# Kernel optimization log

Hardware: AMD Instinct MI355X
Metric: run time of the kernel (lower is better)

Reference implementation:

```python
import jax, jax.numpy as jnp
import numpy as np

NUM_HEADS = 8
NUM_GROUPS = 32
EPS = 1e-5


def setup_inputs() -> dict:
    key = jax.random.key(0)
    ks = jax.random.split(key, 5)
    B, C, H, W = 8, 512, 32, 32
    x = jax.random.normal(ks[0], (B, C, H, W), dtype=jnp.float32)
    norm_w = jnp.ones((C,), dtype=jnp.float32)
    norm_b = jnp.zeros((C,), dtype=jnp.float32)
    qkv_w = jax.random.normal(ks[1], (3 * C, C), dtype=jnp.float32) * (1.0 / np.sqrt(C))
    qkv_b = jax.random.normal(ks[2], (3 * C,), dtype=jnp.float32) * 0.02
    proj_w = jax.random.normal(ks[3], (C, C), dtype=jnp.float32) * (1.0 / np.sqrt(C))
    proj_b = jax.random.normal(ks[4], (C,), dtype=jnp.float32) * 0.02
    return {"x": x, "norm_w": norm_w, "norm_b": norm_b,
            "qkv_w": qkv_w, "qkv_b": qkv_b, "proj_w": proj_w, "proj_b": proj_b}


def _group_norm(x, w, b):
    # x: [B, C, T]; normalize over (C//G, T) per group
    B, C, T = x.shape
    xg = x.reshape(B, NUM_GROUPS, (C // NUM_GROUPS) * T)
    mean = xg.mean(axis=-1, keepdims=True)
    var = xg.var(axis=-1, keepdims=True)
    xn = ((xg - mean) * jax.lax.rsqrt(var + EPS)).reshape(B, C, T)
    return xn * w[None, :, None] + b[None, :, None]


def reference(x, norm_w, norm_b, qkv_w, qkv_b, proj_w, proj_b):
    B, C, H, W = x.shape
    T = H * W
    x3 = x.reshape(B, C, T)
    h = _group_norm(x3, norm_w, norm_b)
    # 1x1 conv == channel matmul: [B, 3C, T]
    qkv = jnp.einsum('oc,bct->bot', qkv_w, h) + qkv_b[None, :, None]
    nh = NUM_HEADS
    ch = C // nh
    qkv = qkv.reshape(B * nh, 3 * ch, T)
    q, k, v = jnp.split(qkv, 3, axis=1)  # each [B*nh, ch, T]
    scale = 1.0 / np.sqrt(np.sqrt(ch))
    w = jnp.einsum('bct,bcs->bts', q * scale, k * scale)  # [B*nh, T, T]
    w = jax.nn.softmax(w, axis=-1)
    a = jnp.einsum('bts,bcs->bct', w, v).reshape(B, C, T)
    out = jnp.einsum('oc,bct->bot', proj_w, a) + proj_b[None, :, None]
    return (x3 + out).reshape(B, C, H, W)
```

## Files before the change

kernel.cpp:

```cpp
#include <hip/hip_runtime.h>
#include <stdint.h>

typedef short v8s __attribute__((ext_vector_type(8)));
typedef float v4f __attribute__((ext_vector_type(4)));

#define MFMA(a, b, c) __builtin_amdgcn_mfma_f32_16x16x32_bf16((a), (b), (c), 0, 0, 0)

__device__ __forceinline__ short f2bf(float f) {
  union { float f; uint32_t u; } v; v.f = f;
  uint32_t r = v.u + 0x7fffu + ((v.u >> 16) & 1u);
  return (short)(r >> 16);
}

__device__ __forceinline__ uint32_t pack2(float a, float b) {
  union { float f; uint32_t u; } ua, ub; ua.f = a; ub.f = b;
  return __builtin_amdgcn_perm(ub.u, ua.u, 0x07060302u);
}

__device__ __forceinline__ void gload16(const void* g, void* l) {
  __builtin_amdgcn_global_load_lds((const __attribute__((address_space(1))) void*)g,
                                   (__attribute__((address_space(3))) void*)l,
                                   16, 0, 0);
}

__global__ __launch_bounds__(256) void prep_gn_kernel(
    const float* __restrict__ qkvw, const float* __restrict__ qkvb,
    const float* __restrict__ projw,
    short* __restrict__ Wq, short* __restrict__ Wp, float* __restrict__ bias2,
    const float* __restrict__ x, const float* __restrict__ gw,
    const float* __restrict__ gb, short* __restrict__ hT) {
  __shared__ float red[8];
  __shared__ short tile[16 * 1032];
  int tid = threadIdx.x;
  if (blockIdx.x >= 256) {
    int idx = (blockIdx.x - 256) * 256 + tid;
    if (idx < 1536 * 512) {
      int r = idx >> 9, c = idx & 511;
      int sec = r >> 9;
      int rr = r & 511;
      int nh = rr >> 6, cc = rr & 63;
      int o = nh * 192 + sec * 64 + cc;
      Wq[idx] = f2bf(qkvw[o * 512 + c]);
      if (c == 0) bias2[r] = qkvb[o];
    } else {
      int j = idx - 1536 * 512;
      if (j < 512 * 512) Wp[j] = f2bf(projw[j]);
    }
    return;
  }
  int b = blockIdx.x >> 5, g = blockIdx.x & 31;
  const float* xg = x + (b * 512 + g * 16) * 1024;
  float s = 0.f, ss = 0.f;
#pragma unroll
  for (int r = 0; r < 16; ++r) {
    float4 v = *(const float4*)(xg + r * 1024 + tid * 4);
    s += v.x + v.y + v.z + v.w;
    ss += v.x * v.x + v.y * v.y + v.z * v.z + v.w * v.w;
  }
#pragma unroll
  for (int off = 32; off > 0; off >>= 1) {
    s += __shfl_xor(s, off, 64);
    ss += __shfl_xor(ss, off, 64);
  }
  if ((tid & 63) == 0) { red[tid >> 6] = s; red[4 + (tid >> 6)] = ss; }
  __syncthreads();
  float S = red[0] + red[1] + red[2] + red[3];
  float SS = red[4] + red[5] + red[6] + red[7];
  float mean = S * (1.f / 16384.f);
  float var = SS * (1.f / 16384.f) - mean * mean;
  float inv = rsqrtf(var + 1e-5f);
#pragma unroll
  for (int r = 0; r < 16; ++r) {
    int c = g * 16 + r;
    float a = inv * gw[c];
    float bb = gb[c] - mean * a;
    float4 v = *(const float4*)(xg + r * 1024 + tid * 4);
    short* tr = tile + r * 1032 + tid * 4;
    tr[0] = f2bf(fmaf(v.x, a, bb));
    tr[1] = f2bf(fmaf(v.y, a, bb));
    tr[2] = f2bf(fmaf(v.z, a, bb));
    tr[3] = f2bf(fmaf(v.w, a, bb));
  }
  __syncthreads();
  int r = tid & 15, tq = tid >> 4;
  int c = g * 16 + r;
  short* dst = hT + b * 1024 * 512 + c;
  const short* src = tile + r * 1032;
#pragma unroll
  for (int i = 0; i < 64; ++i) {
    int t = i * 16 + tq;
    dst[t * 512] = src[t];
  }
}

__device__ __forceinline__ void gemm_k512_b64(
    const short* __restrict__ Ag, const short* __restrict__ Bg,
    short* lA, short* lB, int wid, int lane, v4f acc[4][4]) {
  int wr = (wid >> 1) * 64, wc = (wid & 1) * 64;
  int c16 = lane & 15, q = lane >> 4;
  int srow = lane >> 3;
  int sw = ((lane & 7) ^ srow) * 8;
  const short* gaw = Ag + (wid * 32 + srow) * 512 + sw;
  const short* gbw = Bg + (wid * 32 + srow) * 512 + sw;
  short* lAw = lA + wid * 2048;
  short* lBw = lB + wid * 2048;
  int pc0 = (q ^ (c16 & 7)) * 8;
  int pc1 = ((4 + q) ^ (c16 & 7)) * 8;
  for (int kt = 0; kt < 8; ++kt) {
    int k0 = kt * 64;
#pragma unroll
    for (int t = 0; t < 4; ++t)
      gload16(gaw + t * 8 * 512 + k0, lAw + t * 512);
#pragma unroll
    for (int t = 0; t < 4; ++t)
      gload16(gbw + t * 8 * 512 + k0, lBw + t * 512);
    __syncthreads();
#pragma unroll
    for (int ks = 0; ks < 2; ++ks) {
      int pc = ks ? pc1 : pc0;
      v8s af[4], bf[4];
#pragma unroll
      for (int i = 0; i < 4; ++i)
        af[i] = *(const v8s*)(lA + (wr + i * 16 + c16) * 64 + pc);
#pragma unroll
      for (int j = 0; j < 4; ++j)
        bf[j] = *(const v8s*)(lB + (wc + j * 16 + c16) * 64 + pc);
#pragma unroll
      for (int i = 0; i < 4; ++i)
#pragma unroll
        for (int j = 0; j < 4; ++j)
          acc[i][j] = MFMA(af[i], bf[j], acc[i][j]);
    }
    __syncthreads();
  }
}

__global__ __launch_bounds__(256) void qkv_gemm_kernel(
    const short* __restrict__ hT, const short* __restrict__ Wq,
    const float* __restrict__ bias2,
    short* __restrict__ Qb, short* __restrict__ Kb, short* __restrict__ Vb) {
  __shared__ __align__(16) short smem[17408];
  short* lA = smem;
  short* lB = smem + 8192;
  short* vt = smem;
  int bm = blockIdx.x & 63, bo = blockIdx.x >> 6;
  int tid = threadIdx.x, wid = tid >> 6, lane = tid & 63;
  int wr = (wid >> 1) * 64, wc = (wid & 1) * 64;
  int q = lane >> 4, c16 = lane & 15;
  v4f acc[4][4];
#pragma unroll
  for (int i = 0; i < 4; ++i)
#pragma unroll
    for (int j = 0; j < 4; ++j) acc[i][j] = (v4f){0.f, 0.f, 0.f, 0.f};
  gemm_k512_b64(hT + bm * 128 * 512, Wq + bo * 128 * 512, lA, lB, wid, lane, acc);
  float bv[4];
#pragma unroll
  for (int j = 0; j < 4; ++j) bv[j] = bias2[bo * 128 + wc + j * 16 + c16];
  if (bo < 8) {
    short* dst = (bo < 4) ? Qb : Kb;
    float sc = (bo < 4) ? 0.18033688f : 1.f;
#pragma unroll
    for (int j = 0; j < 4; ++j) {
      int ol = wc + j * 16 + c16;
#pragma unroll
      for (int i = 0; i < 4; ++i)
#pragma unroll
        for (int rr = 0; rr < 4; ++rr) {
          int nl = wr + i * 16 + q * 4 + rr;
          vt[nl * 136 + ol] = f2bf((acc[i][j][rr] + bv[j]) * sc);
        }
    }
    __syncthreads();
    int chunk = tid & 15, row0 = tid >> 4;
    int obase = (bo & 3) * 128 + chunk * 8;
    int nh = obase >> 6, cc = obase & 63;
#pragma unroll
    for (int ps = 0; ps < 8; ++ps) {
      int row = row0 + ps * 16;
      int n = bm * 128 + row;
      int b_ = n >> 10, t = n & 1023;
      *(v8s*)(dst + b_ * 524288 + nh * 65536 + t * 64 + cc) =
          *(const v8s*)(vt + row * 136 + chunk * 8);
    }
  } else {
#pragma unroll
    for (int j = 0; j < 4; ++j) {
      int ol = wc + j * 16 + c16;
#pragma unroll
      for (int i = 0; i < 4; ++i)
#pragma unroll
        for (int rr = 0; rr < 4; ++rr) {
          int nl = wr + i * 16 + q * 4 + rr;
          vt[ol * 136 + nl] = f2bf(acc[i][j][rr] + bv[j]);
        }
    }
    __syncthreads();
    int ol = tid >> 1, hf = tid & 1;
    int ovg = (bo - 8) * 128 + ol;
    const short* src = vt + ol * 136 + hf * 64;
    short* dstv = Vb + ovg * 8192 + bm * 128 + hf * 64;
#pragma unroll
    for (int m = 0; m < 8; ++m)
      *(v8s*)(dstv + m * 8) = *(const v8s*)(src + m * 8);
  }
}

__global__ __launch_bounds__(512, 4) void attn_kernel(
    const short* __restrict__ Qb, const short* __restrict__ Kb,
    const short* __restrict__ Vb, short* __restrict__ aT) {
  __shared__ __align__(16) short lds[35840];
  int hb = blockIdx.x >> 3, tt = blockIdx.x & 7;
  int b = hb >> 3, nh = hb & 7;
  int tid = threadIdx.x, wid = tid >> 6, lane = tid & 63;
  int chunk = wid >> 2, w4 = wid & 3;
  int q = lane >> 4, c16 = lane & 15;
  const short* Qh = Qb + hb * 65536;
  const short* Kh = Kb + hb * 65536;
  const short* Vh = Vb + nh * 64 * 8192 + b * 1024;
  int t0 = tt * 128 + w4 * 32;
  int sbase = chunk * 512;
  short* Kst = lds + chunk * 4096;
  short* Vst = lds + 8192 + chunk * 4096;
  short* pw = lds + 16384 + wid * 2432;
  v8s qf[2][2];
#pragma unroll
  for (int i = 0; i < 2; ++i)
#pragma unroll
    for (int kk = 0; kk < 2; ++kk)
      qf[i][kk] = *(const v8s*)(Qh + (t0 + i * 16 + c16) * 64 + kk * 32 + q * 8);
  v4f of[2][4];
  float lsum[2] = {0.f, 0.f};
#pragma unroll
  for (int i = 0; i < 2; ++i)
#pragma unroll
    for (int j = 0; j < 4; ++j) of[i][j] = (v4f){0.f, 0.f, 0.f, 0.f};
  int sidx0 = w4 * 128 + lane;
  int sidx1 = w4 * 128 + 64 + lane;
  int r0 = sidx0 >> 3, m0 = (sidx0 & 7) ^ (r0 & 7);
  int r1 = sidx1 >> 3, m1 = (sidx1 & 7) ^ (r1 & 7);
#pragma unroll 1
  for (int st = 0; st < 8; ++st) {
    int s0 = sbase + st * 64;
    gload16(Kh + (s0 + r0) * 64 + m0 * 8, Kst + (w4 * 128) * 8);
    gload16(Kh + (s0 + r1) * 64 + m1 * 8, Kst + (w4 * 128 + 64) * 8);
    gload16(Vh + r0 * 8192 + s0 + m0 * 8, Vst + (w4 * 128) * 8);
    gload16(Vh + r1 * 8192 + s0 + m1 * 8, Vst + (w4 * 128 + 64) * 8);
    __syncthreads();
    v8s kf[4][2];
#pragma unroll
    for (int j = 0; j < 4; ++j) {
      int row = j * 16 + c16;
#pragma unroll
      for (int kk = 0; kk < 2; ++kk) {
        int pc = (kk * 4 + q) ^ (c16 & 7);
        kf[j][kk] = *(const v8s*)(Kst + row * 64 + pc * 8);
      }
    }
#pragma unroll
    for (int j = 0; j < 4; ++j) {
      v4f s0v = (v4f){0.f, 0.f, 0.f, 0.f};
      s0v = MFMA(kf[j][0], qf[0][0], s0v);
      s0v = MFMA(kf[j][1], qf[0][1], s0v);
      v4f s1v = (v4f){0.f, 0.f, 0.f, 0.f};
      s1v = MFMA(kf[j][0], qf[1][0], s1v);
      s1v = MFMA(kf[j][1], qf[1][1], s1v);
      float p00 = __builtin_amdgcn_exp2f(s0v[0]);
      float p01 = __builtin_amdgcn_exp2f(s0v[1]);
      float p02 = __builtin_amdgcn_exp2f(s0v[2]);
      float p03 = __builtin_amdgcn_exp2f(s0v[3]);
      lsum[0] += (p00 + p01) + (p02 + p03);
      uint2 pk0;
      pk0.x = pack2(p00, p01);
      pk0.y = pack2(p02, p03);
      *(uint2*)(pw + c16 * 76 + j * 16 + q * 4) = pk0;
      float p10 = __builtin_amdgcn_exp2f(s1v[0]);
      float p11 = __builtin_amdgcn_exp2f(s1v[1]);
      float p12 = __builtin_amdgcn_exp2f(s1v[2]);
      float p13 = __builtin_amdgcn_exp2f(s1v[3]);
      lsum[1] += (p10 + p11) + (p12 + p13);
      uint2 pk1;
      pk1.x = pack2(p10, p11);
      pk1.y = pack2(p12, p13);
      *(uint2*)(pw + (16 + c16) * 76 + j * 16 + q * 4) = pk1;
    }
    v8s vf[4][2];
#pragma unroll
    for (int j = 0; j < 4; ++j) {
      int row = j * 16 + c16;
#pragma unroll
      for (int kk = 0; kk < 2; ++kk) {
        int pc = (kk * 4 + q) ^ (c16 & 7);
        vf[j][kk] = *(const v8s*)(Vst + row * 64 + pc * 8);
      }
    }
    asm volatile("s_waitcnt lgkmcnt(0)" ::: "memory");
    v8s pa[2][2];
#pragma unroll
    for (int i = 0; i < 2; ++i)
#pragma unroll
      for (int kk = 0; kk < 2; ++kk)
        pa[i][kk] = *(const v8s*)(pw + (i * 16 + c16) * 76 + kk * 32 + q * 8);
#pragma unroll
    for (int i = 0; i < 2; ++i)
#pragma unroll
      for (int j = 0; j < 4; ++j) {
        of[i][j] = MFMA(pa[i][0], vf[j][0], of[i][j]);
        of[i][j] = MFMA(pa[i][1], vf[j][1], of[i][j]);
      }
    __syncthreads();
  }
#pragma unroll
  for (int i = 0; i < 2; ++i) {
    lsum[i] += __shfl_xor(lsum[i], 16, 64);
    lsum[i] += __shfl_xor(lsum[i], 32, 64);
  }
  float* ex = (float*)(lds + 16384) + w4 * 2144;
  __syncthreads();
  if (chunk == 1) {
#pragma unroll
    for (int i = 0; i < 2; ++i) {
#pragma unroll
      for (int j = 0; j < 4; ++j)
#pragma unroll
        for (int rr = 0; rr < 4; ++rr)
          ex[(i * 16 + q * 4 + rr) * 66 + j * 16 + c16] = of[i][j][rr];
      if (q == 0) ex[2112 + i * 16 + c16] = lsum[i];
    }
  }
  __syncthreads();
  if (chunk == 0) {
    short* base = aT + b * 1024 * 512 + nh * 64;
#pragma unroll
    for (int i = 0; i < 2; ++i)
#pragma unroll
      for (int rr = 0; rr < 4; ++rr) {
        int row = i * 16 + q * 4 + rr;
        float inv = 1.f / (__shfl(lsum[i], q * 4 + rr, 64) + ex[2112 + row]);
        int t = t0 + row;
#pragma unroll
        for (int j = 0; j < 4; ++j) {
          float v = (of[i][j][rr] + ex[row * 66 + j * 16 + c16]) * inv;
          base[t * 512 + j * 16 + c16] = f2bf(v);
        }
      }
  }
}

__global__ __launch_bounds__(256) void proj_gemm_kernel(
    const short* __restrict__ Wp, const short* __restrict__ aT,
    const float* __restrict__ pbias, const float* __restrict__ x,
    float* __restrict__ out) {
  __shared__ __align__(16) short smem[16384];
  short* lA = smem;
  short* lB = smem + 8192;
  int bm = blockIdx.x & 3, bn = blockIdx.x >> 2;
  int tid = threadIdx.x, wid = tid >> 6, lane = tid & 63;
  int wr = (wid >> 1) * 64, wc = (wid & 1) * 64;
  int q = lane >> 4, c16 = lane & 15;
  v4f acc[4][4];
#pragma unroll
  for (int i = 0; i < 4; ++i)
#pragma unroll
    for (int j = 0; j < 4; ++j) acc[i][j] = (v4f){0.f, 0.f, 0.f, 0.f};
  gemm_k512_b64(Wp + bm * 128 * 512, aT + bn * 128 * 512, lA, lB, wid, lane, acc);
  int colOff[4];
#pragma unroll
  for (int j = 0; j < 4; ++j) {
    int n = bn * 128 + wc + j * 16 + c16;
    colOff[j] = (n >> 10) * 524288 + (n & 1023);
  }
#pragma unroll
  for (int i = 0; i < 4; ++i)
#pragma unroll
    for (int rr = 0; rr < 4; ++rr) {
      int o = bm * 128 + wr + i * 16 + q * 4 + rr;
      float bs = pbias[o];
      int ro = o * 1024;
#pragma unroll
      for (int j = 0; j < 4; ++j) {
        int a = colOff[j] + ro;
        out[a] = acc[i][j][rr] + bs + x[a];
      }
    }
}

extern "C" void kernel_launch(void* const* d_in, const int* in_sizes, int n_in,
                              void* d_out, int out_size, void* d_ws, size_t ws_size,
                              hipStream_t stream) {
  const float* x = (const float*)d_in[0];
  const float* nw = (const float*)d_in[1];
  const float* nb = (const float*)d_in[2];
  const float* qkvw = (const float*)d_in[3];
  const float* qkvb = (const float*)d_in[4];
  const float* projw = (const float*)d_in[5];
  const float* projb = (const float*)d_in[6];
  float* out = (float*)d_out;
  char* w = (char*)d_ws;
  short* hT = (short*)(w);
  short* aT = (short*)(w + 8388608);
  short* Qb = (short*)(w + 16777216);
  short* Kb = (short*)(w + 25165824);
  short* Vb = (short*)(w + 33554432);
  short* Wq2 = (short*)(w + 41943040);
  short* Wp2 = (short*)(w + 43515904);
  float* b2 = (float*)(w + 44040192);

  hipLaunchKernelGGL(prep_gn_kernel, dim3(4352), dim3(256), 0, stream,
                     qkvw, qkvb, projw, Wq2, Wp2, b2, x, nw, nb, hT);
  hipLaunchKernelGGL(qkv_gemm_kernel, dim3(768), dim3(256), 0, stream,
                     hT, Wq2, b2, Qb, Kb, Vb);
  hipLaunchKernelGGL(attn_kernel, dim3(512), dim3(512), 0, stream, Qb, Kb, Vb, aT);
  hipLaunchKernelGGL(proj_gemm_kernel, dim3(256), dim3(256), 0, stream,
                     Wp2, aT, projb, x, out);
}
```

Measured before the change: 160.4 us.

## Cache x in registers, vectorize transposed hT stores, and remap attention block order

The group-norm kernel now keeps the 16 float4 loads of x in registers instead of reading them from global memory a second time for normalization. The transposed write of hT now stores four channels at once with 8-byte vector stores instead of scalar 2-byte stores. The attention kernel's block index is remapped so consecutive blocks take different head/batch pairs, which changes how work is placed across compute units and caches. Holding 64 floats per thread raises register pressure in the norm kernel.

```diff
diff --git a/kernel.cpp b/kernel.cpp
--- a/kernel.cpp
+++ b/kernel.cpp
@@ -2,6 +2,7 @@
 #include <stdint.h>
 
 typedef short v8s __attribute__((ext_vector_type(8)));
+typedef short v4s __attribute__((ext_vector_type(4)));
 typedef float v4f __attribute__((ext_vector_type(4)));
 
 #define MFMA(a, b, c) __builtin_amdgcn_mfma_f32_16x16x32_bf16((a), (b), (c), 0, 0, 0)
@@ -50,12 +51,13 @@
   }
   int b = blockIdx.x >> 5, g = blockIdx.x & 31;
   const float* xg = x + (b * 512 + g * 16) * 1024;
+  float4 v[16];
   float s = 0.f, ss = 0.f;
 #pragma unroll
   for (int r = 0; r < 16; ++r) {
-    float4 v = *(const float4*)(xg + r * 1024 + tid * 4);
-    s += v.x + v.y + v.z + v.w;
-    ss += v.x * v.x + v.y * v.y + v.z * v.z + v.w * v.w;
+    v[r] = *(const float4*)(xg + r * 1024 + tid * 4);
+    s += v[r].x + v[r].y + v[r].z + v[r].w;
+    ss += v[r].x * v[r].x + v[r].y * v[r].y + v[r].z * v[r].z + v[r].w * v[r].w;
   }
 #pragma unroll
   for (int off = 32; off > 0; off >>= 1) {
@@ -74,22 +76,22 @@
     int c = g * 16 + r;
     float a = inv * gw[c];
     float bb = gb[c] - mean * a;
-    float4 v = *(const float4*)(xg + r * 1024 + tid * 4);
     short* tr = tile + r * 1032 + tid * 4;
-    tr[0] = f2bf(fmaf(v.x, a, bb));
-    tr[1] = f2bf(fmaf(v.y, a, bb));
-    tr[2] = f2bf(fmaf(v.z, a, bb));
-    tr[3] = f2bf(fmaf(v.w, a, bb));
+    tr[0] = f2bf(fmaf(v[r].x, a, bb));
+    tr[1] = f2bf(fmaf(v[r].y, a, bb));
+    tr[2] = f2bf(fmaf(v[r].z, a, bb));
+    tr[3] = f2bf(fmaf(v[r].w, a, bb));
   }
   __syncthreads();
-  int r = tid & 15, tq = tid >> 4;
-  int c = g * 16 + r;
-  short* dst = hT + b * 1024 * 512 + c;
-  const short* src = tile + r * 1032;
-#pragma unroll
-  for (int i = 0; i < 64; ++i) {
-    int t = i * 16 + tq;
-    dst[t * 512] = src[t];
+  int cq = tid & 3, tq = tid >> 2;
+  int c4 = cq * 4;
+  short* dst = hT + b * 1024 * 512 + g * 16 + c4;
+#pragma unroll
+  for (int i = 0; i < 16; ++i) {
+    int t = i * 64 + tq;
+    v4s val = {tile[(c4 + 0) * 1032 + t], tile[(c4 + 1) * 1032 + t],
+               tile[(c4 + 2) * 1032 + t], tile[(c4 + 3) * 1032 + t]};
+    *(v4s*)(dst + t * 512) = val;
   }
 }
 
@@ -209,7 +211,9 @@
     const short* __restrict__ Qb, const short* __restrict__ Kb,
     const short* __restrict__ Vb, short* __restrict__ aT) {
   __shared__ __align__(16) short lds[35840];
-  int hb = blockIdx.x >> 3, tt = blockIdx.x & 7;
+  int idx = blockIdx.x;
+  int hb = (idx & 7) * 8 + (idx >> 6);
+  int tt = (idx >> 3) & 7;
   int b = hb >> 3, nh = hb & 7;
   int tid = threadIdx.x, wid = tid >> 6, lane = tid & 63;
   int chunk = wid >> 2, w4 = wid & 3;
```

Result: faster. 157.3 us (-2.0%).
